# Kernel tuning notes

Measured on AMD Instinct MI355X. Metric: run time of the kernel, lower is better.

Reference implementation:

```python
import jax, jax.numpy as jnp
import numpy as np

B, N, NNZ = 8, 1024, 1_048_576
F_IN, F_OUT = 64, 64
EPS = 1e-10


def mlp(x, W1, b1, W2, b2):
    # Linear-ReLU-Linear-ReLU, matches nn.Sequential in the torch module
    h = jax.nn.relu(x @ W1 + b1)
    return jax.nn.relu(h @ W2 + b2)


def setup_inputs() -> dict:
    key = jax.random.key(0)
    ks = jax.random.split(key, 16)
    s1 = 1.0 / np.sqrt(F_IN)
    s2 = 1.0 / np.sqrt(F_OUT)
    return {
        "x": jax.random.normal(ks[0], (B, N, F_IN), dtype=jnp.float32),
        "W_val": jax.random.normal(ks[1], (NNZ, F_OUT), dtype=jnp.float32),
        "e_b": jax.random.randint(ks[2], (NNZ,), 0, B, dtype=jnp.int32),
        "e_i": jax.random.randint(ks[3], (NNZ,), 0, N, dtype=jnp.int32),
        "e_j": jax.random.randint(ks[4], (NNZ,), 0, N, dtype=jnp.int32),
        "e_k": jax.random.randint(ks[5], (NNZ,), 0, N, dtype=jnp.int32),
        # n_func_3 params
        "W1": jax.random.normal(ks[6], (F_IN, F_OUT), dtype=jnp.float32) * s1,
        "b1": jnp.zeros((F_OUT,), dtype=jnp.float32),
        "W2": jax.random.normal(ks[7], (F_OUT, F_OUT), dtype=jnp.float32) * s2,
        "b2": jnp.zeros((F_OUT,), dtype=jnp.float32),
        # n_self_func params
        "Ws1": jax.random.normal(ks[8], (F_IN, F_OUT), dtype=jnp.float32) * s1,
        "bs1": jnp.zeros((F_OUT,), dtype=jnp.float32),
        "Ws2": jax.random.normal(ks[9], (F_OUT, F_OUT), dtype=jnp.float32) * s2,
        "bs2": jnp.zeros((F_OUT,), dtype=jnp.float32),
    }


def reference(x, W_val, e_b, e_i, e_j, e_k, W1, b1, W2, b2, Ws1, bs1, Ws2, bs2):
    # --- forward_sparse, order=3, norm=True ---
    # normalization of binary A over dims (2..order) -> 1/deg(b, i)
    seg = e_b.astype(jnp.int32) * N + e_i.astype(jnp.int32)
    deg = jax.ops.segment_sum(jnp.ones((NNZ,), x.dtype), seg, num_segments=B * N)
    a_val = 1.0 / (deg[seg] + EPS)                      # [nnz]

    x1 = mlp(x, W1, b1, W2, b2)                         # [B, N, F_OUT]

    # gather node features at hyperedge tails, multiply across orders
    tp = a_val[:, None] * W_val                         # [nnz, F_OUT]
    tp = tp * x1[e_b, e_k] * x1[e_b, e_j]               # i=0 -> last index, i=1 -> index 2

    # scatter-accumulate to hyperedge head nodes (index_put_ accumulate=True)
    x_new = jnp.zeros_like(x1).at[e_b, e_i].add(tp)     # [B, N, F_OUT]

    # x2 += n_self_func(x)
    x_new = x_new + mlp(x, Ws1, bs1, Ws2, bs2)
    return x_new
```

## Files before the change

### kernel.cpp

```cpp
#include <hip/hip_runtime.h>

#define BN 8192
#define NP 1024
#define NF 64
#define NSEG 8192
#define CAP 256
#define NB 256
#define EPB 4096
#define OVF_MAX 4096

typedef float f32x4 __attribute__((ext_vector_type(4)));

__global__ __launch_bounds__(256) void count_kernel(
    const float* __restrict__ x,
    const float* __restrict__ W1, const float* __restrict__ b1,
    const float* __restrict__ W2, const float* __restrict__ b2,
    const float* __restrict__ Ws1, const float* __restrict__ bs1,
    const float* __restrict__ Ws2, const float* __restrict__ bs2,
    const int* __restrict__ eb, const int* __restrict__ ei,
    int* __restrict__ counts,
    float* __restrict__ x1, float* __restrict__ out, int nnz)
{
    __shared__ int hist[NSEG];
    if ((int)blockIdx.x < NB) {
        const int t = threadIdx.x;
        #pragma unroll
        for (int q = 0; q < 8; ++q)
            *(int4*)(hist + (q * 256 + t) * 4) = make_int4(0, 0, 0, 0);
        __syncthreads();
        const int base = blockIdx.x * EPB;
        #pragma unroll
        for (int q = 0; q < 4; ++q) {
            const int e0 = base + q * 1024 + t * 4;
            if (e0 < nnz) {
                const int4 b4 = *(const int4*)(eb + e0);
                const int4 i4 = *(const int4*)(ei + e0);
                atomicAdd(&hist[b4.x * NP + i4.x], 1);
                atomicAdd(&hist[b4.y * NP + i4.y], 1);
                atomicAdd(&hist[b4.z * NP + i4.z], 1);
                atomicAdd(&hist[b4.w * NP + i4.w], 1);
            }
        }
        __syncthreads();
        int* row = counts + (size_t)blockIdx.x * NSEG;
        #pragma unroll
        for (int q = 0; q < 8; ++q) {
            const int idx = (q * 256 + t) * 4;
            *(int4*)(row + idx) = *(const int4*)(hist + idx);
        }
    } else {
        const int row = ((int)blockIdx.x - NB) * 4 + (threadIdx.x >> 6);
        const int t = threadIdx.x & 63;
        const float xv = x[(size_t)row * NF + t];
        float a1 = b1[t], a2 = bs1[t];
        #pragma unroll 8
        for (int c = 0; c < NF; ++c) {
            const float xc = __shfl(xv, c);
            a1 = fmaf(xc, W1[c * NF + t], a1);
            a2 = fmaf(xc, Ws1[c * NF + t], a2);
        }
        const float h1 = fmaxf(a1, 0.f), h2 = fmaxf(a2, 0.f);
        float o1 = b2[t], o2 = bs2[t];
        #pragma unroll 8
        for (int c = 0; c < NF; ++c) {
            o1 = fmaf(__shfl(h1, c), W2[c * NF + t], o1);
            o2 = fmaf(__shfl(h2, c), Ws2[c * NF + t], o2);
        }
        x1[(size_t)row * NF + t]  = fmaxf(o1, 0.f);
        out[(size_t)row * NF + t] = fmaxf(o2, 0.f);
    }
}

__global__ __launch_bounds__(256) void scan_kernel(
    const int* __restrict__ counts,
    int* __restrict__ offs, int* __restrict__ deg, int* __restrict__ ovf_cnt)
{
    const int s = blockIdx.x * 256 + threadIdx.x;
    int run = 0;
    #pragma unroll 16
    for (int b = 0; b < NB; ++b) {
        const int v = counts[(size_t)b * NSEG + s];
        offs[(size_t)b * NSEG + s] = run;
        run += v;
    }
    deg[s] = run;
    if (s == 0) *ovf_cnt = 0;
}

__global__ __launch_bounds__(256) void scatter_kernel(
    const int* __restrict__ eb, const int* __restrict__ ei,
    const int* __restrict__ ej, const int* __restrict__ ek,
    const int* __restrict__ offs,
    int2* __restrict__ rec, int* __restrict__ ovf_cnt, int4* __restrict__ ovf,
    int nnz)
{
    __shared__ int cur[NSEG];
    const int t = threadIdx.x;
    const int* row = offs + (size_t)blockIdx.x * NSEG;
    #pragma unroll
    for (int q = 0; q < 8; ++q) {
        const int idx = (q * 256 + t) * 4;
        *(int4*)(cur + idx) = *(const int4*)(row + idx);
    }
    __syncthreads();
    const int base = blockIdx.x * EPB;
    #pragma unroll
    for (int q = 0; q < 4; ++q) {
        const int e0 = base + q * 1024 + t * 4;
        if (e0 < nnz) {
            const int4 b4 = *(const int4*)(eb + e0);
            const int4 i4 = *(const int4*)(ei + e0);
            const int4 j4 = *(const int4*)(ej + e0);
            const int4 k4 = *(const int4*)(ek + e0);
            const int segs[4] = {b4.x * NP + i4.x, b4.y * NP + i4.y,
                                 b4.z * NP + i4.z, b4.w * NP + i4.w};
            const int jks[4]  = {(j4.x << 10) | k4.x, (j4.y << 10) | k4.y,
                                 (j4.z << 10) | k4.z, (j4.w << 10) | k4.w};
            #pragma unroll
            for (int c = 0; c < 4; ++c) {
                const int pos = atomicAdd(&cur[segs[c]], 1);
                if (pos < CAP) {
                    rec[(size_t)segs[c] * CAP + pos] = make_int2(e0 + c, jks[c]);
                } else {
                    const int o = atomicAdd(ovf_cnt, 1);
                    if (o < OVF_MAX) ovf[o] = make_int4(segs[c], e0 + c, jks[c], 0);
                }
            }
        }
    }
}

__global__ __launch_bounds__(256, 8) void gather_kernel(
    const f32x4* __restrict__ Wv4, const f32x4* __restrict__ x14,
    const int* __restrict__ deg, const int2* __restrict__ rec,
    const int* __restrict__ ovf_cnt, const int4* __restrict__ ovf,
    f32x4* __restrict__ out4)
{
    __shared__ int2 srec[4][CAP + 4];
    const int w    = threadIdx.x >> 6;
    const int lane = threadIdx.x & 63;
    const int seg  = blockIdx.x * 4 + w;
    const int b    = seg >> 10;
    const int dtrue = deg[seg];
    const int cnt  = min(dtrue, CAP);
    const int cnt4 = (cnt + 3) & ~3;

    for (int i = lane; i < cnt; i += 64)
        srec[w][i] = rec[(size_t)seg * CAP + i];
    if (lane < cnt4 - cnt)
        srec[w][cnt + lane] = make_int2(0, 0);

    const int sub = lane >> 4;
    const int c16 = lane & 15;
    const f32x4* __restrict__ x1b = x14 + ((size_t)b << 10) * 16;

    f32x4 acc = {0.f, 0.f, 0.f, 0.f};
    #pragma unroll 2
    for (int it = 0; it < cnt4; it += 4) {
        const int idx = it + sub;
        const float m = (idx < cnt) ? 1.f : 0.f;
        const int2 r = srec[w][idx];
        const int j = (r.y >> 10) & 1023, k = r.y & 1023;
        const f32x4 wv = __builtin_nontemporal_load(Wv4 + (size_t)(unsigned)r.x * 16 + c16);
        const f32x4 xj = x1b[j * 16 + c16];
        const f32x4 xk = x1b[k * 16 + c16];
        acc += (m * wv) * (xj * xk);
    }

    const int novf = min(ovf_cnt[0], OVF_MAX);
    if (novf > 0) {
        for (int o = 0; o < novf; ++o) {
            const int4 r = ovf[o];
            if (r.x == seg) {
                const float m = (sub == 0) ? 1.f : 0.f;
                const int j = (r.z >> 10) & 1023, k = r.z & 1023;
                const f32x4 wv = Wv4[(size_t)(unsigned)r.y * 16 + c16];
                acc += (m * wv) * (x1b[j * 16 + c16] * x1b[k * 16 + c16]);
            }
        }
    }

    #pragma unroll
    for (int mm = 16; mm < 64; mm <<= 1) {
        acc.x += __shfl_xor(acc.x, mm);
        acc.y += __shfl_xor(acc.y, mm);
        acc.z += __shfl_xor(acc.z, mm);
        acc.w += __shfl_xor(acc.w, mm);
    }

    if (sub == 0) {
        const float a = 1.0f / ((float)dtrue + 1e-10f);
        f32x4 o = out4[(size_t)seg * 16 + c16];
        out4[(size_t)seg * 16 + c16] = o + a * acc;
    }
}

extern "C" void kernel_launch(void* const* d_in, const int* in_sizes, int n_in,
                              void* d_out, int out_size, void* d_ws, size_t ws_size,
                              hipStream_t stream) {
    const float* x   = (const float*)d_in[0];
    const float* Wv  = (const float*)d_in[1];
    const int*   eb  = (const int*)d_in[2];
    const int*   ei  = (const int*)d_in[3];
    const int*   ej  = (const int*)d_in[4];
    const int*   ek  = (const int*)d_in[5];
    const float* W1  = (const float*)d_in[6];
    const float* b1  = (const float*)d_in[7];
    const float* W2  = (const float*)d_in[8];
    const float* b2  = (const float*)d_in[9];
    const float* Ws1 = (const float*)d_in[10];
    const float* bs1 = (const float*)d_in[11];
    const float* Ws2 = (const float*)d_in[12];
    const float* bs2 = (const float*)d_in[13];
    float* out = (float*)d_out;
    const int nnz = in_sizes[2];

    char* ws = (char*)d_ws;
    float* x1    = (float*)ws;
    int* deg     = (int*)(ws + (2 << 20));
    int* ovf_cnt = (int*)(ws + (2 << 20) + (32 << 10));
    int4* ovf    = (int4*)(ws + (2 << 20) + (64 << 10));
    int* counts  = (int*)(ws + (4 << 20));
    int* offs    = (int*)(ws + (12 << 20));
    int2* rec    = (int2*)(ws + (20 << 20));

    count_kernel<<<NB + BN / 4, 256, 0, stream>>>(x, W1, b1, W2, b2, Ws1, bs1, Ws2, bs2,
                                                  eb, ei, counts, x1, out, nnz);
    scan_kernel<<<NSEG / 256, 256, 0, stream>>>(counts, offs, deg, ovf_cnt);
    scatter_kernel<<<NB, 256, 0, stream>>>(eb, ei, ej, ek, offs, rec, ovf_cnt, ovf, nnz);
    gather_kernel<<<NSEG / 4, 256, 0, stream>>>((const f32x4*)Wv, (const f32x4*)x1,
                                                deg, rec, ovf_cnt, ovf, (f32x4*)out);
}
```

Measured before the change: 129.4 us.

## Split column scan into hierarchical three-pass scan and double histogram blocks

The single scan kernel used only 32 blocks, each thread walking serially over all 256 per-block histograms. It becomes a three-pass hierarchical scan: group sums, a prefix over the groups, then per-group offsets, which exposes 16x more threads. The count and scatter phases now use 512 blocks of 2048 edges each instead of 256 blocks of 4096, raising parallelism there as well. In exchange, the histogram and offset arrays double in size (more memory traffic for zeroing and copying the 32KB per-block histograms) and there are two extra kernel launches.

```diff
diff --git a/kernel.cpp b/kernel.cpp
--- a/kernel.cpp
+++ b/kernel.cpp
@@ -5,8 +5,10 @@
 #define NF 64
 #define NSEG 8192
 #define CAP 256
-#define NB 256
-#define EPB 4096
+#define NB 512
+#define EPB 2048
+#define G 32
+#define NG (NB / G)
 #define OVF_MAX 4096
 
 typedef float f32x4 __attribute__((ext_vector_type(4)));
@@ -30,8 +32,8 @@
         __syncthreads();
         const int base = blockIdx.x * EPB;
         #pragma unroll
-        for (int q = 0; q < 4; ++q) {
-            const int e0 = base + q * 1024 + t * 4;
+        for (int q = 0; q < 2; ++q) {
+            const int e0 = base + (q * 256 + t) * 4;
             if (e0 < nnz) {
                 const int4 b4 = *(const int4*)(eb + e0);
                 const int4 i4 = *(const int4*)(ei + e0);
@@ -71,20 +73,47 @@
     }
 }
 
-__global__ __launch_bounds__(256) void scan_kernel(
-    const int* __restrict__ counts,
-    int* __restrict__ offs, int* __restrict__ deg, int* __restrict__ ovf_cnt)
+__global__ __launch_bounds__(256) void scan_a_kernel(
+    const int* __restrict__ counts, int* __restrict__ gsum)
+{
+    const int tid = blockIdx.x * 256 + threadIdx.x;
+    const int g = tid >> 13, s = tid & (NSEG - 1);
+    const int* col = counts + (size_t)g * G * NSEG + s;
+    int sum = 0;
+    #pragma unroll
+    for (int i = 0; i < G; ++i) sum += col[(size_t)i * NSEG];
+    gsum[g * NSEG + s] = sum;
+}
+
+__global__ __launch_bounds__(256) void scan_b_kernel(
+    const int* __restrict__ gsum, int* __restrict__ gbase,
+    int* __restrict__ deg, int* __restrict__ ovf_cnt)
 {
     const int s = blockIdx.x * 256 + threadIdx.x;
     int run = 0;
-    #pragma unroll 16
-    for (int b = 0; b < NB; ++b) {
-        const int v = counts[(size_t)b * NSEG + s];
-        offs[(size_t)b * NSEG + s] = run;
-        run += v;
+    #pragma unroll
+    for (int g = 0; g < NG; ++g) {
+        gbase[g * NSEG + s] = run;
+        run += gsum[g * NSEG + s];
     }
     deg[s] = run;
     if (s == 0) *ovf_cnt = 0;
+}
+
+__global__ __launch_bounds__(256) void scan_c_kernel(
+    const int* __restrict__ counts, const int* __restrict__ gbase,
+    int* __restrict__ offs)
+{
+    const int tid = blockIdx.x * 256 + threadIdx.x;
+    const int g = tid >> 13, s = tid & (NSEG - 1);
+    int run = gbase[g * NSEG + s];
+    const int* col = counts + (size_t)g * G * NSEG + s;
+    int* ocol = offs + (size_t)g * G * NSEG + s;
+    #pragma unroll
+    for (int i = 0; i < G; ++i) {
+        ocol[(size_t)i * NSEG] = run;
+        run += col[(size_t)i * NSEG];
+    }
 }
 
 __global__ __launch_bounds__(256) void scatter_kernel(
@@ -105,8 +134,8 @@
     __syncthreads();
     const int base = blockIdx.x * EPB;
     #pragma unroll
-    for (int q = 0; q < 4; ++q) {
-        const int e0 = base + q * 1024 + t * 4;
+    for (int q = 0; q < 2; ++q) {
+        const int e0 = base + (q * 256 + t) * 4;
         if (e0 < nnz) {
             const int4 b4 = *(const int4*)(eb + e0);
             const int4 i4 = *(const int4*)(ei + e0);
@@ -220,13 +249,17 @@
     int* deg     = (int*)(ws + (2 << 20));
     int* ovf_cnt = (int*)(ws + (2 << 20) + (32 << 10));
     int4* ovf    = (int4*)(ws + (2 << 20) + (64 << 10));
+    int* gsum    = (int*)(ws + (2 << 20) + (128 << 10));
+    int* gbase   = (int*)(ws + (2 << 20) + (640 << 10));
     int* counts  = (int*)(ws + (4 << 20));
-    int* offs    = (int*)(ws + (12 << 20));
-    int2* rec    = (int2*)(ws + (20 << 20));
+    int* offs    = (int*)(ws + (20 << 20));
+    int2* rec    = (int2*)(ws + (36 << 20));
 
     count_kernel<<<NB + BN / 4, 256, 0, stream>>>(x, W1, b1, W2, b2, Ws1, bs1, Ws2, bs2,
                                                   eb, ei, counts, x1, out, nnz);
-    scan_kernel<<<NSEG / 256, 256, 0, stream>>>(counts, offs, deg, ovf_cnt);
+    scan_a_kernel<<<NG * NSEG / 256, 256, 0, stream>>>(counts, gsum);
+    scan_b_kernel<<<NSEG / 256, 256, 0, stream>>>(gsum, gbase, deg, ovf_cnt);
+    scan_c_kernel<<<NG * NSEG / 256, 256, 0, stream>>>(counts, gbase, offs);
     scatter_kernel<<<NB, 256, 0, stream>>>(eb, ei, ej, ek, offs, rec, ovf_cnt, ovf, nnz);
     gather_kernel<<<NSEG / 4, 256, 0, stream>>>((const f32x4*)Wv, (const f32x4*)x1,
                                                 deg, rec, ovf_cnt, ovf, (f32x4*)out);
```

New measurement: 129.9 us. Within noise of the previous version (+0.4%).
